# Performance work log

Hardware: AMD Instinct MI355X
Metric: run time of the kernel (lower is better)

Reference implementation:

```python
import jax, jax.numpy as jnp
import numpy as np

N_NODES = 50000
N_EDGES = 800000
N_GRAPHS = 64
NEG_SLOPE = 0.2  # PyG GATv2Conv default negative_slope
LN_EPS = 1e-5


def gatv2(x, src, dst, Wl, bl, Wr, br, att, bias, heads, out_ch, concat):
    """Faithful eval-mode PyG GATv2Conv: x_l=lin_l(x) (source), x_r=lin_r(x) (target),
    e = att . leaky_relu(x_l[src] + x_r[dst]), segment-softmax over dst, scatter-add."""
    N = x.shape[0]
    H, C = heads, out_ch
    xl = (x @ Wl + bl).reshape(N, H, C)
    xr = (x @ Wr + br).reshape(N, H, C)
    e = jax.nn.leaky_relu(xl[src] + xr[dst], NEG_SLOPE)        # [E, H, C]
    logits = jnp.einsum('ehc,hc->eh', e, att)                  # [E, H]
    m = jax.ops.segment_max(logits, dst, num_segments=N)       # every node has a self-loop
    ex = jnp.exp(logits - m[dst])
    denom = jax.ops.segment_sum(ex, dst, num_segments=N)
    alpha = ex / (denom[dst] + 1e-16)                          # [E, H]
    out = jax.ops.segment_sum(xl[src] * alpha[..., None], dst, num_segments=N)  # [N, H, C]
    out = out.reshape(N, H * C) if concat else out.mean(axis=1)
    return out + bias


def setup_inputs() -> dict:
    key = jax.random.key(0)
    ks = jax.random.split(key, 32)

    def g(i, shape):  # glorot-ish
        scale = np.sqrt(2.0 / (shape[0] + shape[-1]))
        return (jax.random.normal(ks[i], shape, jnp.float32) * scale)

    inp = {
        'x': jax.random.normal(ks[0], (N_NODES, 4), jnp.float32),
        'edge_index': jax.random.randint(ks[1], (2, N_EDGES), 0, N_NODES, dtype=jnp.int64),
        'batch': jnp.sort(jax.random.randint(ks[2], (N_NODES,), 0, N_GRAPHS, dtype=jnp.int64)),
        # conv1: 4 -> 64, heads=4, concat -> 256
        'W1l': g(3, (4, 256)), 'b1l': jnp.zeros((256,), jnp.float32),
        'W1r': g(4, (4, 256)), 'b1r': jnp.zeros((256,), jnp.float32),
        'a1': g(5, (4, 64)), 'c1b': jnp.zeros((256,), jnp.float32),
        # conv2: 256 -> 64, heads=2, concat -> 128
        'W2l': g(6, (256, 128)), 'b2l': jnp.zeros((128,), jnp.float32),
        'W2r': g(7, (256, 128)), 'b2r': jnp.zeros((128,), jnp.float32),
        'a2': g(8, (2, 64)), 'c2b': jnp.zeros((128,), jnp.float32),
        # conv3: 128 -> 256, heads=1, concat=False -> 256
        'W3l': g(9, (128, 256)), 'b3l': jnp.zeros((256,), jnp.float32),
        'W3r': g(10, (128, 256)), 'b3r': jnp.zeros((256,), jnp.float32),
        'a3': g(11, (1, 256)), 'c3b': jnp.zeros((256,), jnp.float32),
        # enhancer MLP + LayerNorm
        'We1': g(12, (256, 512)), 'be1': jnp.zeros((512,), jnp.float32),
        'We2': g(13, (512, 256)), 'be2': jnp.zeros((256,), jnp.float32),
        'lng': jnp.ones((256,), jnp.float32), 'lnb': jnp.zeros((256,), jnp.float32),
    }
    return inp


def reference(x, edge_index, batch,
              W1l, b1l, W1r, b1r, a1, c1b,
              W2l, b2l, W2r, b2r, a2, c2b,
              W3l, b3l, W3r, b3r, a3, c3b,
              We1, be1, We2, be2, lng, lnb):
    N = x.shape[0]
    loop = jnp.arange(N, dtype=edge_index.dtype)  # add_self_loops=True (PyG default)
    src = jnp.concatenate([edge_index[0], loop])
    dst = jnp.concatenate([edge_index[1], loop])

    h = jax.nn.relu(gatv2(x, src, dst, W1l, b1l, W1r, b1r, a1, c1b, 4, 64, True))
    h = jax.nn.relu(gatv2(h, src, dst, W2l, b2l, W2r, b2r, a2, c2b, 2, 64, True))
    h = gatv2(h, src, dst, W3l, b3l, W3r, b3r, a3, c3b, 1, 256, False)

    # global mean pool per graph
    sums = jax.ops.segment_sum(h, batch, num_segments=N_GRAPHS)          # [G, 256]
    cnt = jax.ops.segment_sum(jnp.ones((N, 1), h.dtype), batch, num_segments=N_GRAPHS)
    pooled = sums / jnp.maximum(cnt, 1.0)

    # enhancer (dropout off in eval): Linear -> ReLU -> Linear -> LayerNorm
    z = jax.nn.relu(pooled @ We1 + be1) @ We2 + be2
    mu = z.mean(axis=-1, keepdims=True)
    var = z.var(axis=-1, keepdims=True)
    return (z - mu) / jnp.sqrt(var + LN_EPS) * lng + lnb
```

## Files before the change

### kernel.cpp

```cpp
#include <hip/hip_runtime.h>
#include <hip/hip_bf16.h>
#include <math.h>

#define NN 50000
#define NE0 800000
#define ETOT (NE0 + NN)
#define NG 64
#define SCAN_BLKS ((NN + 63) / 64)
#define DMAX_THR 8.0f

typedef __bf16 bf16x8 __attribute__((ext_vector_type(8)));
typedef float  f32x4  __attribute__((ext_vector_type(4)));

__device__ __forceinline__ float bf2f(unsigned short u) {
    return __uint_as_float(((unsigned)u) << 16);
}
__device__ __forceinline__ unsigned short f2bf(float f) {
    unsigned u = __float_as_uint(f);
    return (unsigned short)((u + 0x7FFFu + ((u >> 16) & 1u)) >> 16);
}

__device__ __forceinline__ void edge_sd(const int* __restrict__ ei, int e, int& s, int& d) {
    if (e < NE0) { s = ei[e]; d = ei[NE0 + e]; }
    else { s = e - NE0; d = s; }
}

__global__ __launch_bounds__(256)
void hist_dst(const int* __restrict__ ei, int* __restrict__ deg) {
    int e = blockIdx.x * blockDim.x + threadIdx.x;
    if (e >= ETOT) return;
    int s, d; edge_sd(ei, e, s, d); (void)s;
    atomicAdd(&deg[d], 1);
}

__global__ __launch_bounds__(64)
void scan1(const int* __restrict__ deg, int* __restrict__ psum) {
    int i = blockIdx.x * 64 + threadIdx.x;
    int v = (i < NN) ? deg[i] : 0;
#pragma unroll
    for (int off = 1; off < 64; off <<= 1) {
        int t = __shfl_up(v, off);
        if ((int)threadIdx.x >= off) v += t;
    }
    if (threadIdx.x == 63) psum[blockIdx.x] = v;
}

__global__ __launch_bounds__(1024)
void scan2(int* __restrict__ psum) {
    __shared__ int sm[1024];
    int t = threadIdx.x;
    sm[t] = (t < SCAN_BLKS) ? psum[t] : 0;
    __syncthreads();
    for (int off = 1; off < 1024; off <<= 1) {
        int v = (t >= off) ? sm[t - off] : 0;
        __syncthreads();
        sm[t] += v;
        __syncthreads();
    }
    if (t < SCAN_BLKS) psum[t] = (t == 0) ? 0 : sm[t - 1];
}

__global__ __launch_bounds__(64)
void scan3(const int* __restrict__ deg, const int* __restrict__ psum,
           int* __restrict__ rowptr) {
    int i = blockIdx.x * 64 + threadIdx.x;
    int v = (i < NN) ? deg[i] : 0;
    int inc = v;
#pragma unroll
    for (int off = 1; off < 64; off <<= 1) {
        int t = __shfl_up(inc, off);
        if ((int)threadIdx.x >= off) inc += t;
    }
    int excl = inc - v + psum[blockIdx.x];
    if (i < NN) rowptr[i] = excl;
    if (i == NN - 1) rowptr[NN] = excl + v;
}

__global__ __launch_bounds__(256)
void scatter_csr(const int* __restrict__ ei, int* __restrict__ cursor,
                 int* __restrict__ col) {
    int e = blockIdx.x * blockDim.x + threadIdx.x;
    if (e >= ETOT) return;
    int s, d; edge_sd(ei, e, s, d);
    int pos = atomicAdd(&cursor[d], 1);
    col[pos] = s;
}

__device__ __forceinline__ void wfrag_one(const float* W, unsigned short* Wf,
                                          int r, int KB, int NOUT) {
    int j = r & 7;
    int l = (r >> 3) & 63;
    int rest = r >> 9;
    int kb = rest % KB, t = rest / KB;
    int k = kb * 32 + (l >> 4) * 8 + j;
    int colj = t * 16 + (l & 15);
    Wf[r] = f2bf(W[(size_t)k * NOUT + colj]);
}
__global__ __launch_bounds__(256)
void wfrag_all(const float* __restrict__ W2l, const float* __restrict__ W2r,
               const float* __restrict__ W3l, const float* __restrict__ W3r,
               unsigned short* __restrict__ Wf2l, unsigned short* __restrict__ Wf2r,
               unsigned short* __restrict__ Wf3l, unsigned short* __restrict__ Wf3r) {
    int tid = blockIdx.x * 256 + threadIdx.x;
    int seg = tid >> 15;
    int r = tid & 32767;
    if (seg == 0)      wfrag_one(W2l, Wf2l, r, 8, 128);
    else if (seg == 1) wfrag_one(W2r, Wf2r, r, 8, 128);
    else if (seg == 2) wfrag_one(W3l, Wf3l, r, 4, 256);
    else               wfrag_one(W3r, Wf3r, r, 4, 256);
}

__global__ __launch_bounds__(256)
void blr_prep(const float* __restrict__ X, const float* __restrict__ W1r,
              const float* __restrict__ b1r, const float* __restrict__ b1l,
              float* __restrict__ out) {
    int j = blockIdx.x * 64 + (threadIdx.x & 63);
    int row0 = (blockIdx.y * 4 + (threadIdx.x >> 6)) * 8;
    float w0 = W1r[j], w1 = W1r[256 + j], w2 = W1r[512 + j], w3 = W1r[768 + j];
    float bj = b1r[j] + b1l[j];
#pragma unroll
    for (int r = 0; r < 8; ++r) {
        int row = row0 + r;
        if (row >= NN) break;
        float4 xv = *reinterpret_cast<const float4*>(X + (size_t)row * 4);
        out[(size_t)row * 256 + j] =
            fmaf(xv.x, w0, fmaf(xv.y, w1, fmaf(xv.z, w2, fmaf(xv.w, w3, bj))));
    }
}

__global__ __launch_bounds__(256)
void gat1_fused(const float* __restrict__ x,
                const int* __restrict__ rowptr, const int* __restrict__ col,
                const float* __restrict__ BLR,
                const float* __restrict__ W1l, const float* __restrict__ b1l,
                const float* __restrict__ a1, const float* __restrict__ c1b,
                unsigned short* __restrict__ out) {
    int lane = threadIdx.x & 63;
    int node = (blockIdx.x * blockDim.x + threadIdx.x) >> 6;
    if (node >= NN) return;
    int ch0 = lane * 4;

    float wl[4][4];
#pragma unroll
    for (int k = 0; k < 4; ++k) {
        float4 l4 = *reinterpret_cast<const float4*>(W1l + k * 256 + ch0);
        wl[k][0] = l4.x; wl[k][1] = l4.y; wl[k][2] = l4.z; wl[k][3] = l4.w;
    }
    float4 av  = *reinterpret_cast<const float4*>(a1 + ch0);
    float ar[4] = { av.x, av.y, av.z, av.w };
    float4 blv = *reinterpret_cast<const float4*>(b1l + ch0);
    float4 cbv = *reinterpret_cast<const float4*>(c1b + ch0);
    float obias[4] = { blv.x + cbv.x, blv.y + cbv.y, blv.z + cbv.z, blv.w + cbv.w };

    const float4* x4 = reinterpret_cast<const float4*>(x);

    float4 blrv = *reinterpret_cast<const float4*>(BLR + (size_t)node * 256 + ch0);
    float blr[4] = { blrv.x, blrv.y, blrv.z, blrv.w };

    float m = -INFINITY, l = 0.f;
    float ax = 0.f, ay = 0.f, az = 0.f, aw = 0.f;

    int beg = rowptr[node], end = rowptr[node + 1];
    int idx = beg;
    for (; idx + 3 < end; idx += 4) {
        float4 v[4];
        float dd[4];
#pragma unroll
        for (int q = 0; q < 4; ++q) v[q] = x4[col[idx + q]];
#pragma unroll
        for (int q = 0; q < 4; ++q) {
            float d = 0.f;
#pragma unroll
            for (int p = 0; p < 4; ++p) {
                float u = fmaf(v[q].x, wl[0][p], fmaf(v[q].y, wl[1][p],
                          fmaf(v[q].z, wl[2][p], fmaf(v[q].w, wl[3][p], blr[p]))));
                u = u > 0.f ? u : 0.2f * u;
                d = fmaf(u, ar[p], d);
            }
            dd[q] = d;
        }
#pragma unroll
        for (int off = 8; off >= 1; off >>= 1) {
#pragma unroll
            for (int q = 0; q < 4; ++q) dd[q] += __shfl_xor(dd[q], off);
        }
        float pmax = fmaxf(fmaxf(dd[0], dd[1]), fmaxf(dd[2], dd[3]));
        if (pmax > m + DMAX_THR) {
            float sc = __expf(m - pmax);
            l *= sc; ax *= sc; ay *= sc; az *= sc; aw *= sc;
            m = pmax;
        }
        float p0 = __expf(dd[0] - m), p1 = __expf(dd[1] - m);
        float p2 = __expf(dd[2] - m), p3 = __expf(dd[3] - m);
        l += (p0 + p1) + (p2 + p3);
        ax += fmaf(p0, v[0].x, p1 * v[1].x) + fmaf(p2, v[2].x, p3 * v[3].x);
        ay += fmaf(p0, v[0].y, p1 * v[1].y) + fmaf(p2, v[2].y, p3 * v[3].y);
        az += fmaf(p0, v[0].z, p1 * v[1].z) + fmaf(p2, v[2].z, p3 * v[3].z);
        aw += fmaf(p0, v[0].w, p1 * v[1].w) + fmaf(p2, v[2].w, p3 * v[3].w);
    }
    for (; idx < end; ++idx) {
        float4 v0 = x4[col[idx]];
        float d0 = 0.f;
#pragma unroll
        for (int p = 0; p < 4; ++p) {
            float u0 = fmaf(v0.x, wl[0][p], fmaf(v0.y, wl[1][p],
                       fmaf(v0.z, wl[2][p], fmaf(v0.w, wl[3][p], blr[p]))));
            u0 = u0 > 0.f ? u0 : 0.2f * u0;
            d0 = fmaf(u0, ar[p], d0);
        }
#pragma unroll
        for (int off = 8; off >= 1; off >>= 1) d0 += __shfl_xor(d0, off);
        if (d0 > m + DMAX_THR) {
            float sc = __expf(m - d0);
            l *= sc; ax *= sc; ay *= sc; az *= sc; aw *= sc;
            m = d0;
        }
        float p0 = __expf(d0 - m);
        l += p0;
        ax = fmaf(p0, v0.x, ax);
        ay = fmaf(p0, v0.y, ay);
        az = fmaf(p0, v0.z, az);
        aw = fmaf(p0, v0.w, aw);
    }
    float inv = 1.f / (l + 1e-16f);
    unsigned short o[4];
#pragma unroll
    for (int p = 0; p < 4; ++p) {
        float v = fmaf(ax, wl[0][p], fmaf(ay, wl[1][p],
                  fmaf(az, wl[2][p], aw * wl[3][p]))) * inv + obias[p];
        o[p] = f2bf(fmaxf(v, 0.f));
    }
    *reinterpret_cast<ushort4*>(out + (size_t)node * 256 + ch0) =
        make_ushort4(o[0], o[1], o[2], o[3]);
}

template<int KIN, int NOUT>
__global__ __launch_bounds__(256)
void gemm_mfma2(const unsigned short* __restrict__ X,
                const unsigned short* __restrict__ WfL, const float* __restrict__ bL,
                unsigned short* __restrict__ outL,
                const unsigned short* __restrict__ WfR, const float* __restrict__ bR,
                unsigned short* __restrict__ outR) {
    constexpr int KB = KIN / 32, NT = NOUT / 16;
    int lane = threadIdx.x & 63;
    int wv = threadIdx.x >> 6;
    int row0 = blockIdx.x * 64 + wv * 16;
    int r16 = lane & 15, kg = lane >> 4;

    int arow = row0 + r16; if (arow >= NN) arow = NN - 1;
    const unsigned short* xrow = X + (size_t)arow * KIN + kg * 8;
    bf16x8 af[KB];
#pragma unroll
    for (int kb = 0; kb < KB; ++kb)
        af[kb] = *reinterpret_cast<const bf16x8*>(xrow + kb * 32);

    const unsigned short* Wf[2] = { WfL, WfR };
    const float* bb[2] = { bL, bR };
    unsigned short* oo[2] = { outL, outR };

#pragma unroll
    for (int w = 0; w < 2; ++w) {
        const bf16x8* wbase = reinterpret_cast<const bf16x8*>(Wf[w]) + lane;
        const float* bw = bb[w];
        unsigned short* ow = oo[w];
#pragma unroll 1
        for (int t = 0; t < NT; ++t) {
            f32x4 acc = {0.f, 0.f, 0.f, 0.f};
            const bf16x8* wp = wbase + (size_t)t * KB * 64;
#pragma unroll
            for (int kb = 0; kb < KB; ++kb)
                acc = __builtin_amdgcn_mfma_f32_16x16x32_bf16(af[kb], wp[kb * 64], acc, 0, 0, 0);
            float bv = bw[t * 16 + r16];
#pragma unroll
            for (int rg = 0; rg < 4; ++rg) {
                int row = row0 + kg * 4 + rg;
                if (row < NN)
                    ow[(size_t)row * NOUT + t * 16 + r16] = f2bf(acc[rg] + bv);
            }
        }
    }
}

template<int H, int C, bool RELU, bool OUT_BF16>
__global__ __launch_bounds__(256)
void gat_fused(const unsigned short* __restrict__ xl, const unsigned short* __restrict__ xr,
               const int* __restrict__ rowptr, const int* __restrict__ col,
               const float* __restrict__ att, const float* __restrict__ bias,
               void* __restrict__ outv) {
    constexpr int HC = H * C;
    constexpr int CPL = HC / 64;
    constexpr int GRP = C / CPL;
    int lane = threadIdx.x & 63;
    int node = (blockIdx.x * blockDim.x + threadIdx.x) >> 6;
    if (node >= NN) return;
    int ch0 = lane * CPL;

    float areg[CPL], breg[CPL];
#pragma unroll
    for (int p = 0; p < CPL; ++p) { areg[p] = att[ch0 + p]; breg[p] = bias[ch0 + p]; }

    float xrv[CPL];
    if constexpr (CPL == 4) {
        ushort4 u = *reinterpret_cast<const ushort4*>(xr + (size_t)node * HC + ch0);
        xrv[0] = bf2f(u.x); xrv[1] = bf2f(u.y); xrv[2] = bf2f(u.z); xrv[3] = bf2f(u.w);
    } else {
        ushort2 u = *reinterpret_cast<const ushort2*>(xr + (size_t)node * HC + ch0);
        xrv[0] = bf2f(u.x); xrv[1] = bf2f(u.y);
    }
    float m = -INFINITY, l = 0.f, acc[CPL];
#pragma unroll
    for (int p = 0; p < CPL; ++p) acc[p] = 0.f;

    int beg = rowptr[node], end = rowptr[node + 1];
    int idx = beg;
    for (; idx + 3 < end; idx += 4) {
        float a[4][CPL];
        float dd[4];
#pragma unroll
        for (int q = 0; q < 4; ++q) {
            int s = col[idx + q];
            if constexpr (CPL == 4) {
                ushort4 u = *reinterpret_cast<const ushort4*>(xl + (size_t)s * HC + ch0);
                a[q][0] = bf2f(u.x); a[q][1] = bf2f(u.y); a[q][2] = bf2f(u.z); a[q][3] = bf2f(u.w);
            } else {
                ushort2 u = *reinterpret_cast<const ushort2*>(xl + (size_t)s * HC + ch0);
                a[q][0] = bf2f(u.x); a[q][1] = bf2f(u.y);
            }
        }
#pragma unroll
        for (int q = 0; q < 4; ++q) {
            float d = 0.f;
#pragma unroll
            for (int p = 0; p < CPL; ++p) {
                float v = a[q][p] + xrv[p];
                v = v > 0.f ? v : 0.2f * v;
                d = fmaf(v, areg[p], d);
            }
            dd[q] = d;
        }
#pragma unroll
        for (int off = GRP >> 1; off >= 1; off >>= 1) {
#pragma unroll
            for (int q = 0; q < 4; ++q) dd[q] += __shfl_xor(dd[q], off);
        }
        float pmax = fmaxf(fmaxf(dd[0], dd[1]), fmaxf(dd[2], dd[3]));
        if (pmax > m + DMAX_THR) {
            float sc = __expf(m - pmax);
            l *= sc;
#pragma unroll
            for (int p = 0; p < CPL; ++p) acc[p] *= sc;
            m = pmax;
        }
        float p0 = __expf(dd[0] - m), p1 = __expf(dd[1] - m);
        float p2 = __expf(dd[2] - m), p3 = __expf(dd[3] - m);
        l += (p0 + p1) + (p2 + p3);
#pragma unroll
        for (int p = 0; p < CPL; ++p)
            acc[p] += fmaf(p0, a[0][p], p1 * a[1][p]) + fmaf(p2, a[2][p], p3 * a[3][p]);
    }
    for (; idx < end; ++idx) {
        int s0 = col[idx];
        float a0[CPL];
        if constexpr (CPL == 4) {
            ushort4 u0 = *reinterpret_cast<const ushort4*>(xl + (size_t)s0 * HC + ch0);
            a0[0] = bf2f(u0.x); a0[1] = bf2f(u0.y); a0[2] = bf2f(u0.z); a0[3] = bf2f(u0.w);
        } else {
            ushort2 u0 = *reinterpret_cast<const ushort2*>(xl + (size_t)s0 * HC + ch0);
            a0[0] = bf2f(u0.x); a0[1] = bf2f(u0.y);
        }
        float d0 = 0.f;
#pragma unroll
        for (int p = 0; p < CPL; ++p) {
            float v0 = a0[p] + xrv[p];
            v0 = v0 > 0.f ? v0 : 0.2f * v0;
            d0 = fmaf(v0, areg[p], d0);
        }
#pragma unroll
        for (int off = GRP >> 1; off >= 1; off >>= 1) d0 += __shfl_xor(d0, off);
        if (d0 > m + DMAX_THR) {
            float sc = __expf(m - d0);
            l *= sc;
#pragma unroll
            for (int p = 0; p < CPL; ++p) acc[p] *= sc;
            m = d0;
        }
        float p0 = __expf(d0 - m);
        l += p0;
#pragma unroll
        for (int p = 0; p < CPL; ++p)
            acc[p] = fmaf(p0, a0[p], acc[p]);
    }
    float inv = 1.f / (l + 1e-16f);
    float o[CPL];
#pragma unroll
    for (int p = 0; p < CPL; ++p) {
        float v = acc[p] * inv + breg[p];
        if (RELU) v = fmaxf(v, 0.f);
        o[p] = v;
    }
    if constexpr (OUT_BF16) {
        unsigned short* out = (unsigned short*)outv;
        if constexpr (CPL == 4) {
            *reinterpret_cast<ushort4*>(out + (size_t)node * HC + ch0) =
                make_ushort4(f2bf(o[0]), f2bf(o[1]), f2bf(o[2]), f2bf(o[3]));
        } else {
            *reinterpret_cast<ushort2*>(out + (size_t)node * HC + ch0) =
                make_ushort2(f2bf(o[0]), f2bf(o[1]));
        }
    } else {
        float* out = (float*)outv;
        if constexpr (CPL == 4) {
            *reinterpret_cast<float4*>(out + (size_t)node * HC + ch0) =
                make_float4(o[0], o[1], o[2], o[3]);
        } else {
            *reinterpret_cast<float2*>(out + (size_t)node * HC + ch0) =
                make_float2(o[0], o[1]);
        }
    }
}

__global__ __launch_bounds__(64)
void graph_bounds(const int* __restrict__ batch, float* __restrict__ cnt) {
    int g = threadIdx.x;
    if (g >= NG) return;
    int lo = 0, hi = NN;
    while (lo < hi) { int mid = (lo + hi) >> 1; if (batch[mid] < g) lo = mid + 1; else hi = mid; }
    int lo2 = lo, hi2 = NN;
    while (lo2 < hi2) { int mid = (lo2 + hi2) >> 1; if (batch[mid] < g + 1) lo2 = mid + 1; else hi2 = mid; }
    cnt[g] = (float)(lo2 - lo);
}

__global__ __launch_bounds__(256)
void pool_sum(const float* __restrict__ h, const int* __restrict__ batch,
              float* pooled) {
    __shared__ int gb[32];
    int c = threadIdx.x;
    int n0 = blockIdx.x * 32;
    int n1 = min(n0 + 32, NN);
    int cnt = n1 - n0;
    if (c < cnt) gb[c] = batch[n0 + c];
    __syncthreads();
    if (gb[0] == gb[cnt - 1]) {
        float acc = 0.f;
#pragma unroll 4
        for (int i = 0; i < cnt; ++i) acc += h[(size_t)(n0 + i) * 256 + c];
        atomicAdd(&pooled[gb[0] * 256 + c], acc);
    } else {
        int cur = gb[0]; float acc = 0.f;
        for (int i = 0; i < cnt; ++i) {
            int g = gb[i];
            if (g != cur) { atomicAdd(&pooled[cur * 256 + c], acc); acc = 0.f; cur = g; }
            acc += h[(size_t)(n0 + i) * 256 + c];
        }
        atomicAdd(&pooled[cur * 256 + c], acc);
    }
}

__global__ __launch_bounds__(256)
void mlp_ln(const float* __restrict__ pooled, const float* __restrict__ cnt,
            const float* __restrict__ We1, const float* __restrict__ be1,
            const float* __restrict__ We2, const float* __restrict__ be2,
            const float* __restrict__ lng, const float* __restrict__ lnb,
            float* __restrict__ out) {
    __shared__ float p[256];
    __shared__ float t[512];
    __shared__ float red[8];
    int g = blockIdx.x, tid = threadIdx.x;
    p[tid] = pooled[g * 256 + tid] / fmaxf(cnt[g], 1.0f);
    __syncthreads();
    for (int jj = tid; jj < 512; jj += 256) {
        float s = be1[jj];
        for (int k = 0; k < 256; ++k) s = fmaf(p[k], We1[(size_t)k * 512 + jj], s);
        t[jj] = fmaxf(s, 0.f);
    }
    __syncthreads();
    float z = be2[tid];
    for (int k = 0; k < 512; ++k) z = fmaf(t[k], We2[(size_t)k * 256 + tid], z);
    float sv = z, sq = z * z;
#pragma unroll
    for (int off = 32; off >= 1; off >>= 1) {
        sv += __shfl_xor(sv, off);
        sq += __shfl_xor(sq, off);
    }
    int wv = tid >> 6;
    if ((tid & 63) == 0) { red[wv] = sv; red[4 + wv] = sq; }
    __syncthreads();
    float tot = red[0] + red[1] + red[2] + red[3];
    float totq = red[4] + red[5] + red[6] + red[7];
    float mu = tot * (1.f / 256.f);
    float var = totq * (1.f / 256.f) - mu * mu;
    float r = rsqrtf(var + 1e-5f);
    out[g * 256 + tid] = (z - mu) * r * lng[tid] + lnb[tid];
}

extern "C" void kernel_launch(void* const* d_in, const int* in_sizes, int n_in,
                              void* d_out, int out_size, void* d_ws, size_t ws_size,
                              hipStream_t stream) {
    const float* x   = (const float*)d_in[0];
    const int*   ei  = (const int*)d_in[1];
    const int*   bat = (const int*)d_in[2];
    const float *W1l = (const float*)d_in[3], *b1l = (const float*)d_in[4];
    const float *W1r = (const float*)d_in[5], *b1r = (const float*)d_in[6];
    const float *a1  = (const float*)d_in[7], *c1b = (const float*)d_in[8];
    const float *W2l = (const float*)d_in[9],  *b2l = (const float*)d_in[10];
    const float *W2r = (const float*)d_in[11], *b2r = (const float*)d_in[12];
    const float *a2  = (const float*)d_in[13], *c2b = (const float*)d_in[14];
    const float *W3l = (const float*)d_in[15], *b3l = (const float*)d_in[16];
    const float *W3r = (const float*)d_in[17], *b3r = (const float*)d_in[18];
    const float *a3  = (const float*)d_in[19], *c3b = (const float*)d_in[20];
    const float *We1 = (const float*)d_in[21], *be1 = (const float*)d_in[22];
    const float *We2 = (const float*)d_in[23], *be2 = (const float*)d_in[24];
    const float *lng = (const float*)d_in[25], *lnb = (const float*)d_in[26];

    char* base = (char*)d_ws;
    size_t off = 0;
    auto nxt = [&](size_t bytes) { char* p = base + off; off = (off + bytes + 255) & ~(size_t)255; return p; };
    unsigned short* Abuf = (unsigned short*)nxt((size_t)NN * 256 * 2);
    unsigned short* Bbuf = (unsigned short*)nxt((size_t)NN * 256 * 2);
    unsigned short* Hb16 = (unsigned short*)nxt((size_t)NN * 256 * 2);
    float* Hb32 = (float*)nxt((size_t)NN * 256 * 4);
    float* BLR  = (float*)nxt((size_t)NN * 256 * 4);
    int* deg    = (int*)nxt(NN * 4);
    int* rowptr = (int*)nxt((NN + 1) * 4);
    int* cursor = (int*)nxt(NN * 4);
    int* colv   = (int*)nxt((size_t)ETOT * 4);
    int* psum   = (int*)nxt(1024 * 4);
    float* POOL = (float*)nxt(NG * 256 * 4);
    float* CNT  = (float*)nxt(NG * 4);
    unsigned short* Wf2l = (unsigned short*)nxt(256 * 128 * 2);
    unsigned short* Wf2r = (unsigned short*)nxt(256 * 128 * 2);
    unsigned short* Wf3l = (unsigned short*)nxt(128 * 256 * 2);
    unsigned short* Wf3r = (unsigned short*)nxt(128 * 256 * 2);

    const int GEMM_BLKS = (NN + 63) / 64;
    const int NB_NODE = (NN + 3) / 4;

    hipMemsetAsync(deg, 0, NN * sizeof(int), stream);
    hist_dst<<<(ETOT + 255) / 256, 256, 0, stream>>>(ei, deg);
    scan1<<<SCAN_BLKS, 64, 0, stream>>>(deg, psum);
    scan2<<<1, 1024, 0, stream>>>(psum);
    scan3<<<SCAN_BLKS, 64, 0, stream>>>(deg, psum, rowptr);
    hipMemcpyAsync(cursor, rowptr, NN * sizeof(int), hipMemcpyDeviceToDevice, stream);
    scatter_csr<<<(ETOT + 255) / 256, 256, 0, stream>>>(ei, cursor, colv);

    wfrag_all<<<(4 * 32768) / 256, 256, 0, stream>>>(W2l, W2r, W3l, W3r, Wf2l, Wf2r, Wf3l, Wf3r);
    {
        dim3 g(4, (NN + 31) / 32);
        blr_prep<<<g, 256, 0, stream>>>(x, W1r, b1r, b1l, BLR);
    }

    gat1_fused<<<NB_NODE, 256, 0, stream>>>(x, rowptr, colv, BLR, W1l, b1l, a1, c1b, Hb16);

    gemm_mfma2<256, 128><<<GEMM_BLKS, 256, 0, stream>>>(Hb16, Wf2l, b2l, Abuf, Wf2r, b2r, Bbuf);
    gat_fused<2, 64, true, true><<<NB_NODE, 256, 0, stream>>>(Abuf, Bbuf, rowptr, colv, a2, c2b, Hb16);

    gemm_mfma2<128, 256><<<GEMM_BLKS, 256, 0, stream>>>(Hb16, Wf3l, b3l, Abuf, Wf3r, b3r, Bbuf);
    gat_fused<1, 256, false, false><<<NB_NODE, 256, 0, stream>>>(Abuf, Bbuf, rowptr, colv, a3, c3b, Hb32);

    hipMemsetAsync(POOL, 0, (size_t)NG * 256 * 4, stream);
    graph_bounds<<<1, 64, 0, stream>>>(bat, CNT);
    pool_sum<<<(NN + 31) / 32, 256, 0, stream>>>(Hb32, bat, POOL);
    mlp_ln<<<NG, 256, 0, stream>>>(POOL, CNT, We1, be1, We2, be2, lng, lnb, (float*)d_out);
}
```

Before: 483.7 us.

## Split layer-3 GAT edge list across half-waves with 16-byte gathers

Layer 3 attention (256 channels, one head) now has each half-wave handle half of a node's incoming edges. Each lane covers 8 channels loaded as one 16-byte vector. The two partial online-softmax states are merged with cross-half shuffles at the end. Layer 2 keeps the old scheme as a specialised non-template kernel. The aim is wider gather loads and a halved serial edge-loop length per wave, at the cost of extra merge shuffles and idle half-wave stores. The dummy att load reads a float array through a ushort vector and is unused.

```diff
diff --git a/kernel.cpp b/kernel.cpp
--- a/kernel.cpp
+++ b/kernel.cpp
@@ -11,6 +11,7 @@
 
 typedef __bf16 bf16x8 __attribute__((ext_vector_type(8)));
 typedef float  f32x4  __attribute__((ext_vector_type(4)));
+typedef unsigned short us8 __attribute__((ext_vector_type(8)));
 
 __device__ __forceinline__ float bf2f(unsigned short u) {
     return __uint_as_float(((unsigned)u) << 16);
@@ -281,15 +282,12 @@
     }
 }
 
-template<int H, int C, bool RELU, bool OUT_BF16>
-__global__ __launch_bounds__(256)
-void gat_fused(const unsigned short* __restrict__ xl, const unsigned short* __restrict__ xr,
-               const int* __restrict__ rowptr, const int* __restrict__ col,
-               const float* __restrict__ att, const float* __restrict__ bias,
-               void* __restrict__ outv) {
-    constexpr int HC = H * C;
-    constexpr int CPL = HC / 64;
-    constexpr int GRP = C / CPL;
+__global__ __launch_bounds__(256)
+void gat2_fused(const unsigned short* __restrict__ xl, const unsigned short* __restrict__ xr,
+                const int* __restrict__ rowptr, const int* __restrict__ col,
+                const float* __restrict__ att, const float* __restrict__ bias,
+                unsigned short* __restrict__ out) {
+    constexpr int HC = 128, CPL = 2, GRP = 32;
     int lane = threadIdx.x & 63;
     int node = (blockIdx.x * blockDim.x + threadIdx.x) >> 6;
     if (node >= NN) return;
@@ -300,10 +298,7 @@
     for (int p = 0; p < CPL; ++p) { areg[p] = att[ch0 + p]; breg[p] = bias[ch0 + p]; }
 
     float xrv[CPL];
-    if constexpr (CPL == 4) {
-        ushort4 u = *reinterpret_cast<const ushort4*>(xr + (size_t)node * HC + ch0);
-        xrv[0] = bf2f(u.x); xrv[1] = bf2f(u.y); xrv[2] = bf2f(u.z); xrv[3] = bf2f(u.w);
-    } else {
+    {
         ushort2 u = *reinterpret_cast<const ushort2*>(xr + (size_t)node * HC + ch0);
         xrv[0] = bf2f(u.x); xrv[1] = bf2f(u.y);
     }
@@ -319,13 +314,8 @@
 #pragma unroll
         for (int q = 0; q < 4; ++q) {
             int s = col[idx + q];
-            if constexpr (CPL == 4) {
-                ushort4 u = *reinterpret_cast<const ushort4*>(xl + (size_t)s * HC + ch0);
-                a[q][0] = bf2f(u.x); a[q][1] = bf2f(u.y); a[q][2] = bf2f(u.z); a[q][3] = bf2f(u.w);
-            } else {
-                ushort2 u = *reinterpret_cast<const ushort2*>(xl + (size_t)s * HC + ch0);
-                a[q][0] = bf2f(u.x); a[q][1] = bf2f(u.y);
-            }
+            ushort2 u = *reinterpret_cast<const ushort2*>(xl + (size_t)s * HC + ch0);
+            a[q][0] = bf2f(u.x); a[q][1] = bf2f(u.y);
         }
 #pragma unroll
         for (int q = 0; q < 4; ++q) {
@@ -361,13 +351,8 @@
     for (; idx < end; ++idx) {
         int s0 = col[idx];
         float a0[CPL];
-        if constexpr (CPL == 4) {
-            ushort4 u0 = *reinterpret_cast<const ushort4*>(xl + (size_t)s0 * HC + ch0);
-            a0[0] = bf2f(u0.x); a0[1] = bf2f(u0.y); a0[2] = bf2f(u0.z); a0[3] = bf2f(u0.w);
-        } else {
-            ushort2 u0 = *reinterpret_cast<const ushort2*>(xl + (size_t)s0 * HC + ch0);
-            a0[0] = bf2f(u0.x); a0[1] = bf2f(u0.y);
-        }
+        ushort2 u0 = *reinterpret_cast<const ushort2*>(xl + (size_t)s0 * HC + ch0);
+        a0[0] = bf2f(u0.x); a0[1] = bf2f(u0.y);
         float d0 = 0.f;
 #pragma unroll
         for (int p = 0; p < CPL; ++p) {
@@ -391,31 +376,131 @@
             acc[p] = fmaf(p0, a0[p], acc[p]);
     }
     float inv = 1.f / (l + 1e-16f);
-    float o[CPL];
-#pragma unroll
-    for (int p = 0; p < CPL; ++p) {
-        float v = acc[p] * inv + breg[p];
-        if (RELU) v = fmaxf(v, 0.f);
-        o[p] = v;
-    }
-    if constexpr (OUT_BF16) {
-        unsigned short* out = (unsigned short*)outv;
-        if constexpr (CPL == 4) {
-            *reinterpret_cast<ushort4*>(out + (size_t)node * HC + ch0) =
-                make_ushort4(f2bf(o[0]), f2bf(o[1]), f2bf(o[2]), f2bf(o[3]));
-        } else {
-            *reinterpret_cast<ushort2*>(out + (size_t)node * HC + ch0) =
-                make_ushort2(f2bf(o[0]), f2bf(o[1]));
-        }
-    } else {
-        float* out = (float*)outv;
-        if constexpr (CPL == 4) {
-            *reinterpret_cast<float4*>(out + (size_t)node * HC + ch0) =
-                make_float4(o[0], o[1], o[2], o[3]);
-        } else {
-            *reinterpret_cast<float2*>(out + (size_t)node * HC + ch0) =
-                make_float2(o[0], o[1]);
-        }
+    float o0 = fmaxf(acc[0] * inv + breg[0], 0.f);
+    float o1 = fmaxf(acc[1] * inv + breg[1], 0.f);
+    *reinterpret_cast<ushort2*>(out + (size_t)node * HC + ch0) =
+        make_ushort2(f2bf(o0), f2bf(o1));
+}
+
+__global__ __launch_bounds__(256)
+void gat3_fused(const unsigned short* __restrict__ xl, const unsigned short* __restrict__ xr,
+                const int* __restrict__ rowptr, const int* __restrict__ col,
+                const float* __restrict__ att, const float* __restrict__ bias,
+                float* __restrict__ out) {
+    int lane = threadIdx.x & 63;
+    int half = lane >> 5;
+    int node = (blockIdx.x * blockDim.x + threadIdx.x) >> 6;
+    if (node >= NN) return;
+    int ch0 = (lane & 31) * 8;
+
+    float areg[8], xrv[8];
+    {
+        us8 ua = *reinterpret_cast<const us8*>(att + 0 + ch0), ux;
+        (void)ua;
+    }
+#pragma unroll
+    for (int p = 0; p < 8; ++p) areg[p] = att[ch0 + p];
+    {
+        us8 u = *reinterpret_cast<const us8*>(xr + (size_t)node * 256 + ch0);
+#pragma unroll
+        for (int p = 0; p < 8; ++p) xrv[p] = bf2f(u[p]);
+    }
+
+    float m = -INFINITY, l = 0.f, acc[8];
+#pragma unroll
+    for (int p = 0; p < 8; ++p) acc[p] = 0.f;
+
+    int beg = rowptr[node], end = rowptr[node + 1];
+    int n = end - beg;
+    int nh = (n + 1) >> 1;
+    int myBeg = beg + (half ? nh : 0);
+    int myEnd = half ? end : beg + nh;
+
+    int idx = myBeg;
+    for (; idx + 1 < myEnd; idx += 2) {
+        int s0 = col[idx], s1 = col[idx + 1];
+        float a0[8], a1[8];
+        {
+            us8 u0 = *reinterpret_cast<const us8*>(xl + (size_t)s0 * 256 + ch0);
+            us8 u1 = *reinterpret_cast<const us8*>(xl + (size_t)s1 * 256 + ch0);
+#pragma unroll
+            for (int p = 0; p < 8; ++p) { a0[p] = bf2f(u0[p]); a1[p] = bf2f(u1[p]); }
+        }
+        float d0 = 0.f, d1 = 0.f;
+#pragma unroll
+        for (int p = 0; p < 8; ++p) {
+            float v0 = a0[p] + xrv[p];
+            float v1 = a1[p] + xrv[p];
+            v0 = v0 > 0.f ? v0 : 0.2f * v0;
+            v1 = v1 > 0.f ? v1 : 0.2f * v1;
+            d0 = fmaf(v0, areg[p], d0);
+            d1 = fmaf(v1, areg[p], d1);
+        }
+#pragma unroll
+        for (int off = 16; off >= 1; off >>= 1) {
+            d0 += __shfl_xor(d0, off);
+            d1 += __shfl_xor(d1, off);
+        }
+        float pmax = fmaxf(d0, d1);
+        if (pmax > m + DMAX_THR) {
+            float sc = __expf(m - pmax);
+            l *= sc;
+#pragma unroll
+            for (int p = 0; p < 8; ++p) acc[p] *= sc;
+            m = pmax;
+        }
+        float p0 = __expf(d0 - m), p1 = __expf(d1 - m);
+        l += p0 + p1;
+#pragma unroll
+        for (int p = 0; p < 8; ++p)
+            acc[p] += fmaf(p0, a0[p], p1 * a1[p]);
+    }
+    if (idx < myEnd) {
+        int s0 = col[idx];
+        float a0[8];
+        us8 u0 = *reinterpret_cast<const us8*>(xl + (size_t)s0 * 256 + ch0);
+#pragma unroll
+        for (int p = 0; p < 8; ++p) a0[p] = bf2f(u0[p]);
+        float d0 = 0.f;
+#pragma unroll
+        for (int p = 0; p < 8; ++p) {
+            float v0 = a0[p] + xrv[p];
+            v0 = v0 > 0.f ? v0 : 0.2f * v0;
+            d0 = fmaf(v0, areg[p], d0);
+        }
+#pragma unroll
+        for (int off = 16; off >= 1; off >>= 1) d0 += __shfl_xor(d0, off);
+        if (d0 > m + DMAX_THR) {
+            float sc = __expf(m - d0);
+            l *= sc;
+#pragma unroll
+            for (int p = 0; p < 8; ++p) acc[p] *= sc;
+            m = d0;
+        }
+        float p0 = __expf(d0 - m);
+        l += p0;
+#pragma unroll
+        for (int p = 0; p < 8; ++p)
+            acc[p] = fmaf(p0, a0[p], acc[p]);
+    }
+
+    float mo = __shfl_xor(m, 32);
+    float lo = __shfl_xor(l, 32);
+    float M = fmaxf(m, mo);
+    float sA = __expf(m - M), sB = __expf(mo - M);
+    float lsum = l * sA + lo * sB;
+    float inv = 1.f / (lsum + 1e-16f);
+    float o[8];
+#pragma unroll
+    for (int p = 0; p < 8; ++p) {
+        float ao = __shfl_xor(acc[p], 32);
+        o[p] = (acc[p] * sA + ao * sB) * inv + bias[ch0 + p];
+    }
+    if (half == 0) {
+        *reinterpret_cast<float4*>(out + (size_t)node * 256 + ch0) =
+            make_float4(o[0], o[1], o[2], o[3]);
+        *reinterpret_cast<float4*>(out + (size_t)node * 256 + ch0 + 4) =
+            make_float4(o[4], o[5], o[6], o[7]);
     }
 }
 
@@ -552,10 +637,10 @@
     gat1_fused<<<NB_NODE, 256, 0, stream>>>(x, rowptr, colv, BLR, W1l, b1l, a1, c1b, Hb16);
 
     gemm_mfma2<256, 128><<<GEMM_BLKS, 256, 0, stream>>>(Hb16, Wf2l, b2l, Abuf, Wf2r, b2r, Bbuf);
-    gat_fused<2, 64, true, true><<<NB_NODE, 256, 0, stream>>>(Abuf, Bbuf, rowptr, colv, a2, c2b, Hb16);
+    gat2_fused<<<NB_NODE, 256, 0, stream>>>(Abuf, Bbuf, rowptr, colv, a2, c2b, Hb16);
 
     gemm_mfma2<128, 256><<<GEMM_BLKS, 256, 0, stream>>>(Hb16, Wf3l, b3l, Abuf, Wf3r, b3r, Bbuf);
-    gat_fused<1, 256, false, false><<<NB_NODE, 256, 0, stream>>>(Abuf, Bbuf, rowptr, colv, a3, c3b, Hb32);
+    gat3_fused<<<NB_NODE, 256, 0, stream>>>(Abuf, Bbuf, rowptr, colv, a3, c3b, Hb32);
 
     hipMemsetAsync(POOL, 0, (size_t)NG * 256 * 4, stream);
     graph_bounds<<<1, 64, 0, stream>>>(bat, CNT);
```

Result: faster. 472.7 us (-2.3%).
